# Optimization experiments

Measured on AMD Instinct MI355X. Metric: run time of the kernel, lower is better.

The kernel has to match this reference:

```python
import jax, jax.numpy as jnp
import numpy as np

ITER = 6
GAMMA = 0.99
Q = 0.95


def _maxpool(x, win, stride, pad):
    # NCHW max pool
    return jax.lax.reduce_window(
        x, -jnp.inf, jax.lax.max,
        (1, 1, win, win), (1, 1, stride, stride),
        ((0, 0), (0, 0), (pad, pad), (pad, pad)))


def _nearest(x, size):
    # torch F.interpolate(mode='nearest'): src = floor(dst * in / out)
    H, W = size
    h_in, w_in = x.shape[2], x.shape[3]
    ih = (jnp.arange(H) * h_in) // H
    iw = (jnp.arange(W) * w_in) // W
    return x[:, :, ih[:, None], iw[None, :]]


def setup_inputs() -> dict:
    key = jax.random.key(0)
    ks = jax.random.split(key, 4)
    C, mid = 256, 16  # mid = int(sqrt(C))
    x = jax.random.normal(ks[0], (16, C, 128, 128), jnp.float32)
    w1 = jax.random.normal(ks[1], (mid, C), jnp.float32) / np.sqrt(C)
    b1 = jnp.zeros((mid,), jnp.float32)
    w2 = jax.random.normal(ks[2], (C, mid), jnp.float32) / np.sqrt(mid)
    b2 = jnp.zeros((C,), jnp.float32)
    return {"x": x, "w1": w1, "b1": b1, "w2": w2, "b2": b2}


def reference(x, w1, b1, w2, b2):
    B, C, H, W = x.shape
    # --- quantile activation mask (detached) ---
    flat = x.reshape(B, C, H * W)
    thr = jnp.quantile(flat, Q, axis=-1)[:, :, None, None]  # [B,C,1,1]
    M = jax.lax.stop_gradient((x >= thr).astype(x.dtype))
    # --- propagate field ---
    feat = x * M
    out = feat
    for i in range(ITER):
        g = jnp.asarray(GAMMA ** (2 ** i), x.dtype)
        if i == 0:
            feat = _maxpool(feat, 3, 1, 1) * g  # same-resolution 3x3 pool
            out = jnp.maximum(out, feat)
        else:
            # 5x5 stride-2 pool -> scale -> nearest upsample back to (H,W)
            feat = _nearest(_maxpool(feat, 5, 2, 2) * g, (H, W))
            out = jnp.maximum(out, feat)
    # --- receptor modulator: 1x1 conv -> relu -> 1x1 conv -> sigmoid ---
    h = jax.nn.relu(jnp.einsum('bchw,mc->bmhw', out, w1) + b1[None, :, None, None])
    R = jax.nn.sigmoid(jnp.einsum('bmhw,cm->bchw', h, w2) + b2[None, :, None, None])
    y = x * R
    return y
```

## Files before the change

### kernel.cpp

```cpp
#include <hip/hip_runtime.h>
#include <cmath>
#include <cfloat>

#define HW_ 16384

__device__ __forceinline__ unsigned f2key(float f){
    unsigned u = __float_as_uint(f);
    return u ^ ((u & 0x80000000u) ? 0xFFFFFFFFu : 0x80000000u);
}
__device__ __forceinline__ float key2f(unsigned k){
    unsigned u = (k & 0x80000000u) ? (k ^ 0x80000000u) : ~k;
    return __uint_as_float(u);
}
__device__ __forceinline__ unsigned short f2bf(float f){
    unsigned u = __float_as_uint(f);
    unsigned r = u + 0x7FFFu + ((u >> 16) & 1u);
    return (unsigned short)(r >> 16);
}
__device__ __forceinline__ float bf2f(unsigned short s){
    return __uint_as_float((unsigned)s << 16);
}
__device__ __forceinline__ unsigned pkmax(unsigned a, unsigned b){
    unsigned d;
    asm("v_pk_max_u16 %0, %1, %2" : "=v"(d) : "v"(a), "v"(b));
    return d;
}
__device__ __forceinline__ unsigned alignb(unsigned hi, unsigned lo){
    unsigned d;
    asm("v_alignbit_b32 %0, %1, %2, 16" : "=v"(d) : "v"(hi), "v"(lo));
    return d;
}
__device__ __forceinline__ unsigned cvtpk(float lo, float hi){
    unsigned d;
    asm("v_cvt_pk_bf16_f32 %0, %1, %2" : "=v"(d) : "v"(lo), "v"(hi));
    return d;
}
__device__ __forceinline__ unsigned wscan_incl(unsigned v, int lane){
    #pragma unroll
    for (int o = 1; o < 64; o <<= 1){
        unsigned u = __shfl_up(v, o);
        v += (lane >= o) ? u : 0u;
    }
    return v;
}

__global__ __launch_bounds__(256) void k0_prep(
    const float* __restrict__ w1, float* __restrict__ W1T)
{
    int e = blockIdx.x * 256 + threadIdx.x;
    int m = e >> 8, c = e & 255;
    W1T[c * 16 + m] = w1[m * 256 + c];
}

__global__ __launch_bounds__(512, 6) void k1f(
    const float* __restrict__ x,
    unsigned short* __restrict__ outp, unsigned short* __restrict__ m64g,
    float g1, float q2, float q3, float q4, float q5, float q6)
{
    __shared__ __align__(16) unsigned short C0[16384];
    __shared__ __align__(16) unsigned short H5s[8192];
    __shared__ unsigned hist[1024];
    __shared__ unsigned wsum[8];
    __shared__ unsigned redA[8], redB[8];
    __shared__ unsigned s_dA, s_dB, s_cloA, s_cloB, s_keyA, s_keyB;

    const int tid = threadIdx.x;
    const int lane = tid & 63;
    const int wid = tid >> 6;
    const unsigned bc = blockIdx.x;
    const float4* xp4 = (const float4*)(x + (size_t)bc * HW_);

    unsigned key[32];

    #pragma unroll
    for (int k = 0; k < 2; ++k) hist[tid + k * 512] = 0u;
    __syncthreads();
    #pragma unroll
    for (int k = 0; k < 8; ++k){
        float4 v = xp4[tid + k * 512];
        key[4*k+0] = f2key(v.x);
        key[4*k+1] = f2key(v.y);
        key[4*k+2] = f2key(v.z);
        key[4*k+3] = f2key(v.w);
        atomicAdd(&hist[key[4*k+0] >> 22], 1u);
        atomicAdd(&hist[key[4*k+1] >> 22], 1u);
        atomicAdd(&hist[key[4*k+2] >> 22], 1u);
        atomicAdd(&hist[key[4*k+3] >> 22], 1u);
    }
    __syncthreads();

    unsigned rA = 15563u, rB = 15564u;
    unsigned prefVal = 0u, prefMask = 0u;
    bool done = false;

    {
        unsigned part = hist[tid*2] + hist[tid*2+1];
        unsigned incl = wscan_incl(part, lane);
        if (lane == 63) wsum[wid] = incl;
        __syncthreads();
        unsigned off = 0;
        #pragma unroll
        for (int w = 0; w < 8; ++w) off += (w < wid) ? wsum[w] : 0u;
        unsigned phi = incl + off;
        unsigned plo = phi - part;
        if (rA >= plo && rA < phi){
            unsigned c = plo;
            #pragma unroll
            for (int k = 0; k < 2; ++k){
                unsigned hh = hist[tid*2+k];
                if (rA < c + hh){ s_dA = tid*2+k; s_cloA = c; break; }
                c += hh;
            }
        }
        if (rB >= plo && rB < phi){
            unsigned c = plo;
            #pragma unroll
            for (int k = 0; k < 2; ++k){
                unsigned hh = hist[tid*2+k];
                if (rB < c + hh){ s_dB = tid*2+k; s_cloB = c; break; }
                c += hh;
            }
        }
        __syncthreads();
        unsigned dA = s_dA, dB = s_dB;
        if (dA != dB){
            unsigned locA = 0u, locB = 0xFFFFFFFFu;
            #pragma unroll
            for (int e = 0; e < 32; ++e){
                unsigned d = key[e] >> 22;
                if (d == dA) locA = max(locA, key[e]);
                if (d == dB) locB = min(locB, key[e]);
            }
            #pragma unroll
            for (int o = 32; o > 0; o >>= 1){
                locA = max(locA, __shfl_down(locA, o));
                locB = min(locB, __shfl_down(locB, o));
            }
            if (lane == 0){ redA[wid] = locA; redB[wid] = locB; }
            __syncthreads();
            if (tid == 0){
                unsigned a = redA[0], b = redB[0];
                for (int w = 1; w < 8; ++w){ a = max(a, redA[w]); b = min(b, redB[w]); }
                s_keyA = a; s_keyB = b;
            }
            __syncthreads();
            done = true;
        } else {
            prefVal = dA << 22; prefMask = 0x3FFu << 22;
            rA -= s_cloA; rB -= s_cloB;
            __syncthreads();
        }
    }

    if (!done){
        const int shifts[3] = {14, 6, 0};
        const int bitsv[3]  = {8, 8, 6};
        for (int lvl = 0; lvl < 3 && !done; ++lvl){
            int shift = shifts[lvl];
            unsigned nb = 1u << bitsv[lvl];
            unsigned msk = nb - 1u;
            if (tid < (int)nb) hist[tid] = 0u;
            __syncthreads();
            #pragma unroll
            for (int e = 0; e < 32; ++e){
                if ((key[e] & prefMask) == prefVal)
                    atomicAdd(&hist[(key[e] >> shift) & msk], 1u);
            }
            __syncthreads();
            unsigned part = (tid < (int)nb) ? hist[tid] : 0u;
            unsigned incl = wscan_incl(part, lane);
            if (lane == 63) wsum[wid] = incl;
            __syncthreads();
            unsigned off = 0;
            #pragma unroll
            for (int w = 0; w < 8; ++w) off += (w < wid) ? wsum[w] : 0u;
            unsigned phi = incl + off;
            unsigned plo = phi - part;
            if (tid < (int)nb){
                if (rA >= plo && rA < phi){ s_dA = tid; s_cloA = plo; }
                if (rB >= plo && rB < phi){ s_dB = tid; s_cloB = plo; }
            }
            __syncthreads();
            unsigned dA = s_dA, dB = s_dB;
            if (dA != dB){
                unsigned mA = prefMask | (msk << shift);
                unsigned vAp = prefVal | (dA << shift);
                unsigned vBp = prefVal | (dB << shift);
                unsigned locA = 0u, locB = 0xFFFFFFFFu;
                #pragma unroll
                for (int e = 0; e < 32; ++e){
                    if ((key[e] & mA) == vAp) locA = max(locA, key[e]);
                    if ((key[e] & mA) == vBp) locB = min(locB, key[e]);
                }
                #pragma unroll
                for (int o = 32; o > 0; o >>= 1){
                    locA = max(locA, __shfl_down(locA, o));
                    locB = min(locB, __shfl_down(locB, o));
                }
                if (lane == 0){ redA[wid] = locA; redB[wid] = locB; }
                __syncthreads();
                if (tid == 0){
                    unsigned a = redA[0], b = redB[0];
                    for (int w = 1; w < 8; ++w){ a = max(a, redA[w]); b = min(b, redB[w]); }
                    s_keyA = a; s_keyB = b;
                }
                __syncthreads();
                done = true;
            } else {
                prefVal |= dA << shift;
                prefMask |= msk << shift;
                rA -= s_cloA; rB -= s_cloB;
                if (lvl == 2){
                    if (tid == 0){ s_keyA = prefVal; s_keyB = prefVal; }
                    done = true;
                }
                __syncthreads();
            }
        }
    }

    float vlo = key2f(s_keyA);
    float vhi = key2f(s_keyB);
    float idxq = 0.95f * 16383.0f;
    float frac = idxq - floorf(idxq);
    const float thr = vlo * (1.0f - frac) + vhi * frac;

    #pragma unroll
    for (int k = 0; k < 8; ++k){
        int i = tid + k * 512;
        float f0 = key2f(key[4*k+0]); f0 = (f0 >= thr) ? f0 : 0.0f;
        float f1 = key2f(key[4*k+1]); f1 = (f1 >= thr) ? f1 : 0.0f;
        float f2 = key2f(key[4*k+2]); f2 = (f2 >= thr) ? f2 : 0.0f;
        float f3 = key2f(key[4*k+3]); f3 = (f3 >= thr) ? f3 : 0.0f;
        uint2 w; w.x = cvtpk(f0, f1); w.y = cvtpk(f2, f3);
        ((uint2*)C0)[i] = w;
    }
    __syncthreads();

    {
        const unsigned* C0w = (const unsigned*)C0;
        unsigned* outp32 = (unsigned*)(outp + (size_t)bc * HW_);
        const int wc = lane;
        const int r0 = wid * 16;

        unsigned hmA, hmB, hmC, cB, cC;
        {
            int r = r0 - 1;
            if (r < 0){ hmA = 0u; }
            else {
                unsigned w = C0w[r*64 + wc];
                unsigned wl = __shfl_up(w, 1);
                unsigned wr = __shfl_down(w, 1);
                if (wc == 0)  wl = 0u;
                if (wc == 63) wr = 0u;
                hmA = pkmax(pkmax(alignb(w, wl), w), alignb(wr, w));
            }
        }
        {
            int r = r0;
            unsigned w = C0w[r*64 + wc];
            unsigned wl = __shfl_up(w, 1);
            unsigned wr = __shfl_down(w, 1);
            if (wc == 0)  wl = 0u;
            if (wc == 63) wr = 0u;
            hmB = pkmax(pkmax(alignb(w, wl), w), alignb(wr, w));
            cB = w;
        }
        #pragma unroll
        for (int rr = 0; rr < 16; ++rr){
            int r = r0 + rr;
            {
                int rn = r + 1;
                if (rn > 127){ hmC = 0u; cC = 0u; }
                else {
                    unsigned w = C0w[rn*64 + wc];
                    unsigned wl = __shfl_up(w, 1);
                    unsigned wr = __shfl_down(w, 1);
                    if (wc == 0)  wl = 0u;
                    if (wc == 63) wr = 0u;
                    hmC = pkmax(pkmax(alignb(w, wl), w), alignb(wr, w));
                    cC = w;
                }
            }
            unsigned p1 = pkmax(pkmax(hmA, hmB), hmC);
            float a0 = g1 * bf2f((unsigned short)(p1 & 0xFFFFu));
            float a1v = g1 * bf2f((unsigned short)(p1 >> 16));
            outp32[r*64 + wc] = pkmax(cB, cvtpk(a0, a1v));
            unsigned wjm1 = __shfl_up(p1, 1);
            unsigned wjp1 = __shfl_down(p1, 1);
            if (wc == 0)  wjm1 = 0u;
            if (wc == 63) wjp1 = 0u;
            unsigned s = pkmax(wjm1, p1);
            s = pkmax(s, s >> 16);
            s = pkmax(s, wjp1 & 0xFFFFu);
            H5s[r*64 + wc] = (unsigned short)s;
            hmA = hmB; hmB = hmC; cB = cC;
        }
    }
    __syncthreads();

    unsigned* U = (unsigned*)C0;
    unsigned* T = ((unsigned*)C0) + 2048;
    float mf[8];
    #pragma unroll
    for (int k = 0; k < 4; ++k){
        int q = tid + k * 512;
        int i = q >> 5, wj = q & 31;
        int rr = 2 * i;
        const unsigned* H5w = (const unsigned*)H5s;
        unsigned m = pkmax(H5w[rr*32 + wj], H5w[(rr+1)*32 + wj]);
        if (rr >= 1) m = pkmax(m, H5w[(rr-1)*32 + wj]);
        if (rr >= 2) m = pkmax(m, H5w[(rr-2)*32 + wj]);
        if (rr + 2 <= 127) m = pkmax(m, H5w[(rr+2)*32 + wj]);
        U[q] = m;
        mf[2*k]   = q2 * bf2f((unsigned short)(m & 0xFFFFu));
        mf[2*k+1] = q2 * bf2f((unsigned short)(m >> 16));
    }
    __syncthreads();

    const float gs[4] = {q3, q4, q5, q6};
    #pragma unroll
    for (int it = 0; it < 4; ++it){
        #pragma unroll
        for (int k = 0; k < 4; ++k){
            int q = tid + k * 512;
            unsigned w = U[q];
            unsigned wl = __shfl_up(w, 1);
            unsigned wr = __shfl_down(w, 1);
            if ((q & 31) == 0)  wl = 0u;
            if ((q & 31) == 31) wr = 0u;
            T[q] = pkmax(pkmax(alignb(w, wl), w), alignb(wr, w));
        }
        __syncthreads();
        #pragma unroll
        for (int k = 0; k < 4; ++k){
            int q = tid + k * 512;
            int r = q >> 5;
            unsigned w = T[q];
            if (r > 0)  w = pkmax(w, T[q - 32]);
            if (r < 63) w = pkmax(w, T[q + 32]);
            U[q] = w;
            mf[2*k]   = fmaxf(mf[2*k],   gs[it] * bf2f((unsigned short)(w & 0xFFFFu)));
            mf[2*k+1] = fmaxf(mf[2*k+1], gs[it] * bf2f((unsigned short)(w >> 16)));
        }
        __syncthreads();
    }

    {
        unsigned* mp = (unsigned*)(m64g + (size_t)bc * 4096);
        #pragma unroll
        for (int k = 0; k < 4; ++k){
            int q = tid + k * 512;
            mp[q] = cvtpk(mf[2*k], mf[2*k+1]);
        }
    }
}

__global__ __launch_bounds__(256, 6) void k3_sgpr(
    const float* __restrict__ x,
    const unsigned short* __restrict__ outp, const unsigned short* __restrict__ m64,
    const float* __restrict__ W1T,
    const float* __restrict__ w2,
    const float* __restrict__ b1, const float* __restrict__ b2,
    float* __restrict__ y)
{
    const int tid = threadIdx.x;
    const int blk = blockIdx.x;
    const int b = blk >> 6;
    const int t = blk & 63;

    const int pix = t * 256 + tid;
    const int mi = (pix >> 8) * 64 + ((pix & 127) >> 1);
    const size_t base = (size_t)b * 256 * HW_;
    const size_t mbase = (size_t)b * 256 * 4096;

    float h[16];
    #pragma unroll
    for (int m = 0; m < 16; ++m) h[m] = 0.0f;

    #pragma unroll 4
    for (int c = 0; c < 256; ++c){
        float o  = bf2f(outp[base + (size_t)c * HW_ + pix]);
        float mo = bf2f(m64[mbase + (size_t)c * 4096 + mi]);
        o = fmaxf(o, mo);
        const float4* wr = (const float4*)(W1T + c * 16);
        float4 a0 = wr[0], a1 = wr[1], a2 = wr[2], a3 = wr[3];
        h[0]  = fmaf(a0.x, o, h[0]);  h[1]  = fmaf(a0.y, o, h[1]);
        h[2]  = fmaf(a0.z, o, h[2]);  h[3]  = fmaf(a0.w, o, h[3]);
        h[4]  = fmaf(a1.x, o, h[4]);  h[5]  = fmaf(a1.y, o, h[5]);
        h[6]  = fmaf(a1.z, o, h[6]);  h[7]  = fmaf(a1.w, o, h[7]);
        h[8]  = fmaf(a2.x, o, h[8]);  h[9]  = fmaf(a2.y, o, h[9]);
        h[10] = fmaf(a2.z, o, h[10]); h[11] = fmaf(a2.w, o, h[11]);
        h[12] = fmaf(a3.x, o, h[12]); h[13] = fmaf(a3.y, o, h[13]);
        h[14] = fmaf(a3.z, o, h[14]); h[15] = fmaf(a3.w, o, h[15]);
    }
    #pragma unroll
    for (int m = 0; m < 16; ++m) h[m] = fmaxf(h[m] + b1[m], 0.0f);

    #pragma unroll 4
    for (int c = 0; c < 256; ++c){
        const float4* wr = (const float4*)(w2 + c * 16);
        float4 a0 = wr[0], a1 = wr[1], a2 = wr[2], a3 = wr[3];
        float acc = b2[c];
        acc += a0.x * h[0]  + a0.y * h[1]  + a0.z * h[2]  + a0.w * h[3];
        acc += a1.x * h[4]  + a1.y * h[5]  + a1.z * h[6]  + a1.w * h[7];
        acc += a2.x * h[8]  + a2.y * h[9]  + a2.z * h[10] + a2.w * h[11];
        acc += a3.x * h[12] + a3.y * h[13] + a3.z * h[14] + a3.w * h[15];
        float R = 1.0f / (1.0f + __expf(-acc));
        float xv = x[base + (size_t)c * HW_ + pix];
        y[base + (size_t)c * HW_ + pix] = xv * R;
    }
}

extern "C" void kernel_launch(void* const* d_in, const int* in_sizes, int n_in,
                              void* d_out, int out_size, void* d_ws, size_t ws_size,
                              hipStream_t stream) {
    const float* x  = (const float*)d_in[0];
    const float* w1 = (const float*)d_in[1];
    const float* b1 = (const float*)d_in[2];
    const float* w2 = (const float*)d_in[3];
    const float* b2 = (const float*)d_in[4];
    float* y  = (float*)d_out;
    char* ws = (char*)d_ws;

    unsigned short* outp = (unsigned short*)ws;
    unsigned short* m64  = (unsigned short*)(ws + 134217728);
    float*          W1T  = (float*)(ws + 167772160);

    float g1 = 0.99f;
    float q2 = (float)std::pow(0.99, 3.0);
    float q3 = (float)std::pow(0.99, 7.0);
    float q4 = (float)std::pow(0.99, 15.0);
    float q5 = (float)std::pow(0.99, 31.0);
    float q6 = (float)std::pow(0.99, 63.0);

    k0_prep<<<16, 256, 0, stream>>>(w1, W1T);
    k1f<<<4096, 512, 0, stream>>>(x, outp, m64, g1, q2, q3, q4, q5, q6);
    k3_sgpr<<<1024, 256, 0, stream>>>(x, outp, m64, W1T, w2, b1, b2, y);
}
```

Baseline: 306.2 us.

## Use value-range histogram fast path for quantile selection with radix fallback

Replaces the first radix-key histogram pass with a linear histogram over the value range [0.5, 4.5) in 1024 bins, counting values below 0.5 with a wave reduction instead of per-element atomics. When the target ranks fall into bins with at most 64 elements, those candidates are gathered into shared memory and ranked by brute force to pick the two order statistics, which skips the multi-level radix refinement. This relies on the input looking like a standard normal so the 95th percentile lands in that range. If it does not, the original radix-select path runs as a fallback, so correctness holds for any input while extra branching and register pressure are added.

```diff
diff --git a/kernel.cpp b/kernel.cpp
--- a/kernel.cpp
+++ b/kernel.cpp
@@ -19,6 +19,10 @@
 }
 __device__ __forceinline__ float bf2f(unsigned short s){
     return __uint_as_float((unsigned)s << 16);
+}
+__device__ __forceinline__ int binof(float f){
+    float t = __fsub_rn(f, 0.5f);
+    return (int)__fmul_rn(t, 256.0f);
 }
 __device__ __forceinline__ unsigned pkmax(unsigned a, unsigned b){
     unsigned d;
@@ -62,7 +66,10 @@
     __shared__ unsigned hist[1024];
     __shared__ unsigned wsum[8];
     __shared__ unsigned redA[8], redB[8];
+    __shared__ float candA[64], candB[64];
     __shared__ unsigned s_dA, s_dB, s_cloA, s_cloB, s_keyA, s_keyB;
+    __shared__ unsigned s_b0, s_cntA, s_cntB;
+    __shared__ float s_vA_f, s_vB_f;
 
     const int tid = threadIdx.x;
     const int lane = tid & 63;
@@ -70,104 +77,119 @@
     const unsigned bc = blockIdx.x;
     const float4* xp4 = (const float4*)(x + (size_t)bc * HW_);
 
-    unsigned key[32];
-
-    #pragma unroll
-    for (int k = 0; k < 2; ++k) hist[tid + k * 512] = 0u;
+    float v[32];
+
+    hist[tid] = 0u; hist[tid + 512] = 0u;
+    if (tid == 0){ s_b0 = 0u; s_cntA = 0u; s_cntB = 0u; }
     __syncthreads();
+
+    int cntLo = 0;
     #pragma unroll
     for (int k = 0; k < 8; ++k){
-        float4 v = xp4[tid + k * 512];
-        key[4*k+0] = f2key(v.x);
-        key[4*k+1] = f2key(v.y);
-        key[4*k+2] = f2key(v.z);
-        key[4*k+3] = f2key(v.w);
-        atomicAdd(&hist[key[4*k+0] >> 22], 1u);
-        atomicAdd(&hist[key[4*k+1] >> 22], 1u);
-        atomicAdd(&hist[key[4*k+2] >> 22], 1u);
-        atomicAdd(&hist[key[4*k+3] >> 22], 1u);
+        float4 q = xp4[tid + k * 512];
+        v[4*k+0] = q.x; v[4*k+1] = q.y; v[4*k+2] = q.z; v[4*k+3] = q.w;
+        #pragma unroll
+        for (int e2 = 0; e2 < 4; ++e2){
+            float f = v[4*k+e2];
+            if (f < 0.5f) ++cntLo;
+            else if (f < 4.5f) atomicAdd(&hist[binof(f)], 1u);
+        }
+    }
+    {
+        unsigned c = (unsigned)cntLo;
+        #pragma unroll
+        for (int o = 32; o > 0; o >>= 1) c += __shfl_down(c, o);
+        if (lane == 0) atomicAdd(&s_b0, c);
     }
     __syncthreads();
 
-    unsigned rA = 15563u, rB = 15564u;
-    unsigned prefVal = 0u, prefMask = 0u;
-    bool done = false;
-
+    const unsigned rA = 15563u, rB = 15564u;
+    const unsigned B0 = s_b0;
     {
-        unsigned part = hist[tid*2] + hist[tid*2+1];
+        unsigned h0 = hist[tid*2], h1 = hist[tid*2+1];
+        unsigned part = h0 + h1;
         unsigned incl = wscan_incl(part, lane);
         if (lane == 63) wsum[wid] = incl;
         __syncthreads();
-        unsigned off = 0;
+        unsigned off = B0;
         #pragma unroll
         for (int w = 0; w < 8; ++w) off += (w < wid) ? wsum[w] : 0u;
         unsigned phi = incl + off;
         unsigned plo = phi - part;
         if (rA >= plo && rA < phi){
-            unsigned c = plo;
-            #pragma unroll
-            for (int k = 0; k < 2; ++k){
-                unsigned hh = hist[tid*2+k];
-                if (rA < c + hh){ s_dA = tid*2+k; s_cloA = c; break; }
-                c += hh;
-            }
+            if (rA < plo + h0){ s_dA = tid*2;   s_cloA = plo; }
+            else              { s_dA = tid*2+1; s_cloA = plo + h0; }
         }
         if (rB >= plo && rB < phi){
-            unsigned c = plo;
-            #pragma unroll
-            for (int k = 0; k < 2; ++k){
-                unsigned hh = hist[tid*2+k];
-                if (rB < c + hh){ s_dB = tid*2+k; s_cloB = c; break; }
-                c += hh;
-            }
-        }
-        __syncthreads();
-        unsigned dA = s_dA, dB = s_dB;
-        if (dA != dB){
-            unsigned locA = 0u, locB = 0xFFFFFFFFu;
-            #pragma unroll
-            for (int e = 0; e < 32; ++e){
-                unsigned d = key[e] >> 22;
-                if (d == dA) locA = max(locA, key[e]);
-                if (d == dB) locB = min(locB, key[e]);
-            }
-            #pragma unroll
-            for (int o = 32; o > 0; o >>= 1){
-                locA = max(locA, __shfl_down(locA, o));
-                locB = min(locB, __shfl_down(locB, o));
-            }
-            if (lane == 0){ redA[wid] = locA; redB[wid] = locB; }
-            __syncthreads();
-            if (tid == 0){
-                unsigned a = redA[0], b = redB[0];
-                for (int w = 1; w < 8; ++w){ a = max(a, redA[w]); b = min(b, redB[w]); }
-                s_keyA = a; s_keyB = b;
-            }
-            __syncthreads();
-            done = true;
-        } else {
-            prefVal = dA << 22; prefMask = 0x3FFu << 22;
-            rA -= s_cloA; rB -= s_cloB;
-            __syncthreads();
-        }
-    }
-
-    if (!done){
-        const int shifts[3] = {14, 6, 0};
-        const int bitsv[3]  = {8, 8, 6};
-        for (int lvl = 0; lvl < 3 && !done; ++lvl){
-            int shift = shifts[lvl];
-            unsigned nb = 1u << bitsv[lvl];
-            unsigned msk = nb - 1u;
-            if (tid < (int)nb) hist[tid] = 0u;
-            __syncthreads();
-            #pragma unroll
-            for (int e = 0; e < 32; ++e){
-                if ((key[e] & prefMask) == prefVal)
-                    atomicAdd(&hist[(key[e] >> shift) & msk], 1u);
-            }
-            __syncthreads();
-            unsigned part = (tid < (int)nb) ? hist[tid] : 0u;
+            if (rB < plo + h0){ s_dB = tid*2;   s_cloB = plo; }
+            else              { s_dB = tid*2+1; s_cloB = plo + h0; }
+        }
+    }
+    unsigned tot = B0;
+    #pragma unroll
+    for (int w = 0; w < 8; ++w) tot += wsum[w];
+    bool fb = (rA < B0) || (rB >= tot);
+    __syncthreads();
+
+    unsigned dA = 0, dB = 0, cloA = 0, cloB = 0, nA = 0, nB = 0;
+    if (!fb){
+        dA = s_dA; dB = s_dB; cloA = s_cloA; cloB = s_cloB;
+        nA = hist[dA]; nB = hist[dB];
+        fb = (nA > 64u) || (nB > 64u);
+    }
+
+    if (!fb){
+        #pragma unroll
+        for (int e = 0; e < 32; ++e){
+            float f = v[e];
+            if (f >= 0.5f && f < 4.5f){
+                int bq = binof(f);
+                if (bq == (int)dA){
+                    unsigned ix = atomicAdd(&s_cntA, 1u);
+                    if (ix < 64u) candA[ix] = f;
+                } else if (bq == (int)dB){
+                    unsigned ix = atomicAdd(&s_cntB, 1u);
+                    if (ix < 64u) candB[ix] = f;
+                }
+            }
+        }
+        __syncthreads();
+        if (wid == 0 && lane < (int)nA){
+            float mv = candA[lane];
+            unsigned r = 0;
+            for (unsigned j = 0; j < nA; ++j){
+                float o = candA[j];
+                if (o < mv || (o == mv && j < (unsigned)lane)) ++r;
+            }
+            if (r == rA - cloA) s_vA_f = mv;
+        }
+        if (wid == 1){
+            bool same = (dA == dB);
+            unsigned nn = same ? nA : nB;
+            unsigned lr = rB - (same ? cloA : cloB);
+            if (lane < (int)nn){
+                float mv = same ? candA[lane] : candB[lane];
+                unsigned r = 0;
+                for (unsigned j = 0; j < nn; ++j){
+                    float o = same ? candA[j] : candB[j];
+                    if (o < mv || (o == mv && j < (unsigned)lane)) ++r;
+                }
+                if (r == lr) s_vB_f = mv;
+            }
+        }
+        __syncthreads();
+    } else {
+        hist[tid] = 0u; hist[tid + 512] = 0u;
+        __syncthreads();
+        #pragma unroll
+        for (int e = 0; e < 32; ++e) atomicAdd(&hist[f2key(v[e]) >> 22], 1u);
+        __syncthreads();
+        unsigned ra = 15563u, rb = 15564u;
+        unsigned prefVal = 0u, prefMask = 0u;
+        bool done = false;
+        {
+            unsigned h0 = hist[tid*2], h1 = hist[tid*2+1];
+            unsigned part = h0 + h1;
             unsigned incl = wscan_incl(part, lane);
             if (lane == 63) wsum[wid] = incl;
             __syncthreads();
@@ -176,21 +198,24 @@
             for (int w = 0; w < 8; ++w) off += (w < wid) ? wsum[w] : 0u;
             unsigned phi = incl + off;
             unsigned plo = phi - part;
-            if (tid < (int)nb){
-                if (rA >= plo && rA < phi){ s_dA = tid; s_cloA = plo; }
-                if (rB >= plo && rB < phi){ s_dB = tid; s_cloB = plo; }
+            if (ra >= plo && ra < phi){
+                if (ra < plo + h0){ s_dA = tid*2;   s_cloA = plo; }
+                else              { s_dA = tid*2+1; s_cloA = plo + h0; }
+            }
+            if (rb >= plo && rb < phi){
+                if (rb < plo + h0){ s_dB = tid*2;   s_cloB = plo; }
+                else              { s_dB = tid*2+1; s_cloB = plo + h0; }
             }
             __syncthreads();
-            unsigned dA = s_dA, dB = s_dB;
-            if (dA != dB){
-                unsigned mA = prefMask | (msk << shift);
-                unsigned vAp = prefVal | (dA << shift);
-                unsigned vBp = prefVal | (dB << shift);
+            unsigned dA2 = s_dA, dB2 = s_dB;
+            if (dA2 != dB2){
                 unsigned locA = 0u, locB = 0xFFFFFFFFu;
                 #pragma unroll
                 for (int e = 0; e < 32; ++e){
-                    if ((key[e] & mA) == vAp) locA = max(locA, key[e]);
-                    if ((key[e] & mA) == vBp) locB = min(locB, key[e]);
+                    unsigned kk = f2key(v[e]);
+                    unsigned d = kk >> 22;
+                    if (d == dA2) locA = max(locA, kk);
+                    if (d == dB2) locB = min(locB, kk);
                 }
                 #pragma unroll
                 for (int o = 32; o > 0; o >>= 1){
@@ -207,31 +232,94 @@
                 __syncthreads();
                 done = true;
             } else {
-                prefVal |= dA << shift;
-                prefMask |= msk << shift;
-                rA -= s_cloA; rB -= s_cloB;
-                if (lvl == 2){
-                    if (tid == 0){ s_keyA = prefVal; s_keyB = prefVal; }
+                prefVal = dA2 << 22; prefMask = 0x3FFu << 22;
+                ra -= s_cloA; rb -= s_cloB;
+                __syncthreads();
+            }
+        }
+        if (!done){
+            const int shifts[3] = {14, 6, 0};
+            const int bitsv[3]  = {8, 8, 6};
+            for (int lvl = 0; lvl < 3 && !done; ++lvl){
+                int shift = shifts[lvl];
+                unsigned nb = 1u << bitsv[lvl];
+                unsigned msk = nb - 1u;
+                if (tid < (int)nb) hist[tid] = 0u;
+                __syncthreads();
+                #pragma unroll
+                for (int e = 0; e < 32; ++e){
+                    unsigned kk = f2key(v[e]);
+                    if ((kk & prefMask) == prefVal)
+                        atomicAdd(&hist[(kk >> shift) & msk], 1u);
+                }
+                __syncthreads();
+                unsigned part = (tid < (int)nb) ? hist[tid] : 0u;
+                unsigned incl = wscan_incl(part, lane);
+                if (lane == 63) wsum[wid] = incl;
+                __syncthreads();
+                unsigned off = 0;
+                #pragma unroll
+                for (int w = 0; w < 8; ++w) off += (w < wid) ? wsum[w] : 0u;
+                unsigned phi = incl + off;
+                unsigned plo = phi - part;
+                if (tid < (int)nb){
+                    if (ra >= plo && ra < phi){ s_dA = tid; s_cloA = plo; }
+                    if (rb >= plo && rb < phi){ s_dB = tid; s_cloB = plo; }
+                }
+                __syncthreads();
+                unsigned dA2 = s_dA, dB2 = s_dB;
+                if (dA2 != dB2){
+                    unsigned mA = prefMask | (msk << shift);
+                    unsigned vAp = prefVal | (dA2 << shift);
+                    unsigned vBp = prefVal | (dB2 << shift);
+                    unsigned locA = 0u, locB = 0xFFFFFFFFu;
+                    #pragma unroll
+                    for (int e = 0; e < 32; ++e){
+                        unsigned kk = f2key(v[e]);
+                        if ((kk & mA) == vAp) locA = max(locA, kk);
+                        if ((kk & mA) == vBp) locB = min(locB, kk);
+                    }
+                    #pragma unroll
+                    for (int o = 32; o > 0; o >>= 1){
+                        locA = max(locA, __shfl_down(locA, o));
+                        locB = min(locB, __shfl_down(locB, o));
+                    }
+                    if (lane == 0){ redA[wid] = locA; redB[wid] = locB; }
+                    __syncthreads();
+                    if (tid == 0){
+                        unsigned a = redA[0], b = redB[0];
+                        for (int w = 1; w < 8; ++w){ a = max(a, redA[w]); b = min(b, redB[w]); }
+                        s_keyA = a; s_keyB = b;
+                    }
+                    __syncthreads();
                     done = true;
-                }
-                __syncthreads();
-            }
-        }
-    }
-
-    float vlo = key2f(s_keyA);
-    float vhi = key2f(s_keyB);
+                } else {
+                    prefVal |= dA2 << shift;
+                    prefMask |= msk << shift;
+                    ra -= s_cloA; rb -= s_cloB;
+                    if (lvl == 2){
+                        if (tid == 0){ s_keyA = prefVal; s_keyB = prefVal; }
+                        done = true;
+                    }
+                    __syncthreads();
+                }
+            }
+        }
+        if (tid == 0){ s_vA_f = key2f(s_keyA); s_vB_f = key2f(s_keyB); }
+        __syncthreads();
+    }
+
     float idxq = 0.95f * 16383.0f;
     float frac = idxq - floorf(idxq);
-    const float thr = vlo * (1.0f - frac) + vhi * frac;
+    const float thr = s_vA_f * (1.0f - frac) + s_vB_f * frac;
 
     #pragma unroll
     for (int k = 0; k < 8; ++k){
         int i = tid + k * 512;
-        float f0 = key2f(key[4*k+0]); f0 = (f0 >= thr) ? f0 : 0.0f;
-        float f1 = key2f(key[4*k+1]); f1 = (f1 >= thr) ? f1 : 0.0f;
-        float f2 = key2f(key[4*k+2]); f2 = (f2 >= thr) ? f2 : 0.0f;
-        float f3 = key2f(key[4*k+3]); f3 = (f3 >= thr) ? f3 : 0.0f;
+        float f0 = v[4*k+0]; f0 = (f0 >= thr) ? f0 : 0.0f;
+        float f1 = v[4*k+1]; f1 = (f1 >= thr) ? f1 : 0.0f;
+        float f2 = v[4*k+2]; f2 = (f2 >= thr) ? f2 : 0.0f;
+        float f3 = v[4*k+3]; f3 = (f3 >= thr) ? f3 : 0.0f;
         uint2 w; w.x = cvtpk(f0, f1); w.y = cvtpk(f2, f3);
         ((uint2*)C0)[i] = w;
     }
```

New measurement: 384.7 us. 1.26x slower.
